# Performance work log

Measured on AMD Instinct MI355X. Metric: run time of the kernel, lower is better.

## Reference

```python
import jax, jax.numpy as jnp
import numpy as np

B, QN, KN, DIN, DPROJ = 8, 2048, 2048, 1024, 1024

def setup_inputs() -> dict:
    key = jax.random.key(0)
    ks = jax.random.split(key, 10)
    s = 1.0 / np.sqrt(DIN)
    return {
        "query": jax.random.normal(ks[0], (B, QN, DIN), jnp.float32),
        "key": jax.random.normal(ks[1], (B, KN, DIN), jnp.float32),
        "value": jax.random.normal(ks[2], (B, KN, DIN), jnp.float32),
        "mask": jax.random.randint(ks[3], (B, KN), 0, 2, jnp.int32),
        "Wq": jax.random.uniform(ks[4], (DPROJ, DIN), jnp.float32, -s, s),
        "bq": jax.random.uniform(ks[5], (DPROJ,), jnp.float32, -s, s),
        "Wk": jax.random.uniform(ks[6], (DPROJ, DIN), jnp.float32, -s, s),
        "bk": jax.random.uniform(ks[7], (DPROJ,), jnp.float32, -s, s),
        "Wv": jax.random.uniform(ks[8], (DPROJ, DIN), jnp.float32, -s, s),
        "bv": jax.random.uniform(ks[9], (DPROJ,), jnp.float32, -s, s),
    }

def reference(query, key, value, mask, Wq, bq, Wk, bk, Wv, bv):
    pq = jnp.einsum('bqc,dc->bqd', query, Wq) + bq  # (b, qn, dproj)
    pk = jnp.einsum('bkc,dc->bkd', key, Wk) + bk    # (b, kn, dproj)
    pv = jnp.einsum('bkc,dc->bkd', value, Wv) + bv  # (b, kn, dproj)
    scores = jnp.einsum('bqd,bkd->bqk', pq, pk) / jnp.sqrt(jnp.float32(DPROJ))
    m = mask[:, None, :]  # (b, 1, kn) broadcasts over qn
    scores = jnp.where(m == 0, jnp.float32(-1e9), scores)
    attn = jax.nn.softmax(scores, axis=-1)
    attn = attn * m.astype(attn.dtype)  # post-softmax double mask
    ctx = jnp.einsum('bqk,bkd->bqd', attn, pv)
    return (ctx, attn)
```

## Files before the change

### kernel.cpp

```cpp
#include <hip/hip_runtime.h>
#include <hip/hip_bf16.h>


typedef __bf16 bf16;
typedef __bf16 bf16x4 __attribute__((ext_vector_type(4)));
typedef __bf16 bf16x8 __attribute__((ext_vector_type(8)));
typedef float f32x4 __attribute__((ext_vector_type(4)));

#define TILE 128
#define BK 32

__device__ __forceinline__ void gld_lds16(const bf16* g, bf16* l) {
  __builtin_amdgcn_global_load_lds(
      (const __attribute__((address_space(1))) void*)g,
      (__attribute__((address_space(3))) void*)l, 16, 0, 0);
}

__global__ __launch_bounds__(256, 2)
void gemm_f32in(const float* __restrict__ A, int lda,
                const float* __restrict__ Bt, int ldb,
                bf16* __restrict__ C, int ldc,
                const float* __restrict__ bias, int bias_mode, int K)
{
  __shared__ bf16 As[TILE * BK];
  __shared__ bf16 Bs[TILE * BK];
  const int tid = threadIdx.x;
  const int wave = tid >> 6, lane = tid & 63;
  const int wm = (wave >> 1) * 64, wn = (wave & 1) * 64;
  const long m0 = (long)blockIdx.x * TILE;
  const long n0 = (long)blockIdx.y * TILE;

  f32x4 acc[4][4] = {};
  const int fr = lane & 15, fq = lane >> 4;

  for (int k0 = 0; k0 < K; k0 += BK) {
    __syncthreads();
#pragma unroll
    for (int j = 0; j < 4; ++j) {
      int c = j * 256 + tid;
      int row = c >> 3, col = (c & 7) * 4;
      f32x4 av = *(const f32x4*)&A[(m0 + row) * (long)lda + k0 + col];
      f32x4 bv = *(const f32x4*)&Bt[(n0 + row) * (long)ldb + k0 + col];
      bf16x4 ab, bb;
      ab[0] = (bf16)av[0]; ab[1] = (bf16)av[1]; ab[2] = (bf16)av[2]; ab[3] = (bf16)av[3];
      bb[0] = (bf16)bv[0]; bb[1] = (bf16)bv[1]; bb[2] = (bf16)bv[2]; bb[3] = (bf16)bv[3];
      *(bf16x4*)&As[row * BK + col] = ab;
      *(bf16x4*)&Bs[row * BK + col] = bb;
    }
    __syncthreads();

    bf16x8 af[4], bg[4];
#pragma unroll
    for (int i = 0; i < 4; ++i)
      af[i] = *(const bf16x8*)&As[(wm + i * 16 + fr) * BK + fq * 8];
#pragma unroll
    for (int i = 0; i < 4; ++i)
      bg[i] = *(const bf16x8*)&Bs[(wn + i * 16 + fr) * BK + fq * 8];
#pragma unroll
    for (int mi = 0; mi < 4; ++mi)
#pragma unroll
      for (int ni = 0; ni < 4; ++ni)
        acc[mi][ni] = __builtin_amdgcn_mfma_f32_16x16x32_bf16(
            af[mi], bg[ni], acc[mi][ni], 0, 0, 0);
  }

  const int cc = lane & 15, cq = lane >> 4;
#pragma unroll
  for (int mi = 0; mi < 4; ++mi)
#pragma unroll
    for (int ni = 0; ni < 4; ++ni)
#pragma unroll
      for (int r = 0; r < 4; ++r) {
        int row = wm + mi * 16 + cq * 4 + r;
        int col = wn + ni * 16 + cc;
        float v = acc[mi][ni][r];
        if (bias_mode == 1) v += bias[n0 + col];
        else if (bias_mode == 2) v += bias[m0 + row];
        C[(m0 + row) * (long)ldc + (n0 + col)] = (bf16)v;
      }
}

__global__ __launch_bounds__(256, 2)
void gemm_bf16(const bf16* __restrict__ A, int lda, long sA,
               const bf16* __restrict__ Bt, int ldb, long sB,
               float* __restrict__ C, int ldc, long sC,
               int K, float scale)
{
  __shared__ bf16 As[TILE * BK];
  __shared__ bf16 Bs[TILE * BK];
  const int tid = threadIdx.x;
  const int wave = tid >> 6, lane = tid & 63;
  const int wm = (wave >> 1) * 64, wn = (wave & 1) * 64;
  const long m0 = (long)blockIdx.x * TILE;
  const long n0 = (long)blockIdx.y * TILE;
  A  += (long)blockIdx.z * sA;
  Bt += (long)blockIdx.z * sB;
  C  += (long)blockIdx.z * sC;

  f32x4 acc[4][4] = {};

  const int srow = tid >> 2;
  const int scol = (tid & 3) * 8;
  const bf16* Ag0 = A  + (m0 + srow) * (long)lda + scol;
  const bf16* Ag1 = A  + (m0 + 64 + srow) * (long)lda + scol;
  const bf16* Bg0 = Bt + (n0 + srow) * (long)ldb + scol;
  const bf16* Bg1 = Bt + (n0 + 64 + srow) * (long)ldb + scol;
  bf16* Al0 = &As[tid * 8];
  bf16* Al1 = &As[(256 + tid) * 8];
  bf16* Bl0 = &Bs[tid * 8];
  bf16* Bl1 = &Bs[(256 + tid) * 8];

  const int fr = lane & 15, fq = lane >> 4;

  for (int k0 = 0; k0 < K; k0 += BK) {
    __syncthreads();
    gld_lds16(Ag0 + k0, Al0);
    gld_lds16(Ag1 + k0, Al1);
    gld_lds16(Bg0 + k0, Bl0);
    gld_lds16(Bg1 + k0, Bl1);
    __syncthreads();

    bf16x8 af[4], bg[4];
#pragma unroll
    for (int i = 0; i < 4; ++i)
      af[i] = *(const bf16x8*)&As[(wm + i * 16 + fr) * BK + fq * 8];
#pragma unroll
    for (int i = 0; i < 4; ++i)
      bg[i] = *(const bf16x8*)&Bs[(wn + i * 16 + fr) * BK + fq * 8];
#pragma unroll
    for (int mi = 0; mi < 4; ++mi)
#pragma unroll
      for (int ni = 0; ni < 4; ++ni)
        acc[mi][ni] = __builtin_amdgcn_mfma_f32_16x16x32_bf16(
            af[mi], bg[ni], acc[mi][ni], 0, 0, 0);
  }

  const int cc = lane & 15, cq = lane >> 4;
#pragma unroll
  for (int mi = 0; mi < 4; ++mi)
#pragma unroll
    for (int ni = 0; ni < 4; ++ni)
#pragma unroll
      for (int r = 0; r < 4; ++r) {
        int row = wm + mi * 16 + cq * 4 + r;
        int col = wn + ni * 16 + cc;
        C[(m0 + row) * (long)ldc + (n0 + col)] = acc[mi][ni][r] * scale;
      }
}

__global__ __launch_bounds__(256)
void softmax_mask(const int* __restrict__ mask, float* __restrict__ attn,
                  bf16* __restrict__ attnb)
{
  const int row = blockIdx.x;
  const int b = row >> 11;
  float* arow = attn + (long)row * 2048;
  bf16* brow = attnb + (long)row * 2048;
  const int* mrow = mask + (b << 11);
  const int tid = threadIdx.x;
  const int lane = tid & 63, wave = tid >> 6;

  f32x4 s[2];
  int4 mk[2];
  s[0] = *(const f32x4*)&arow[tid * 4];
  s[1] = *(const f32x4*)&arow[1024 + tid * 4];
  mk[0] = *(const int4*)&mrow[tid * 4];
  mk[1] = *(const int4*)&mrow[1024 + tid * 4];
  const int m[8] = {mk[0].x, mk[0].y, mk[0].z, mk[0].w,
                    mk[1].x, mk[1].y, mk[1].z, mk[1].w};

  float mx = -3e38f;
#pragma unroll
  for (int i = 0; i < 8; ++i)
    if (m[i]) mx = fmaxf(mx, s[i >> 2][i & 3]);
#pragma unroll
  for (int off = 32; off > 0; off >>= 1) mx = fmaxf(mx, __shfl_xor(mx, off));
  __shared__ float rmax[4], rsum[4];
  if (lane == 0) rmax[wave] = mx;
  __syncthreads();
  mx = fmaxf(fmaxf(rmax[0], rmax[1]), fmaxf(rmax[2], rmax[3]));

  float e[8], sum = 0.f;
#pragma unroll
  for (int i = 0; i < 8; ++i) {
    e[i] = m[i] ? __expf(s[i >> 2][i & 3] - mx) : 0.f;
    sum += e[i];
  }
#pragma unroll
  for (int off = 32; off > 0; off >>= 1) sum += __shfl_xor(sum, off);
  if (lane == 0) rsum[wave] = sum;
  __syncthreads();
  sum = rsum[0] + rsum[1] + rsum[2] + rsum[3];
  float inv = sum > 0.f ? 1.f / sum : 0.f;

  f32x4 o; bf16x4 ob;
#pragma unroll
  for (int h = 0; h < 2; ++h) {
#pragma unroll
    for (int i = 0; i < 4; ++i) {
      float v = e[h * 4 + i] * inv;
      o[i] = v; ob[i] = (bf16)v;
    }
    *(f32x4*)&arow[h * 1024 + tid * 4] = o;
    *(bf16x4*)&brow[h * 1024 + tid * 4] = ob;
  }
}

extern "C" void kernel_launch(void* const* d_in, const int* in_sizes, int n_in,
                              void* d_out, int out_size, void* d_ws, size_t ws_size,
                              hipStream_t stream)
{
  const float* query = (const float*)d_in[0];
  const float* key   = (const float*)d_in[1];
  const float* value = (const float*)d_in[2];
  const int*   mask  = (const int*)d_in[3];
  const float* Wq = (const float*)d_in[4];
  const float* bq = (const float*)d_in[5];
  const float* Wk = (const float*)d_in[6];
  const float* bk = (const float*)d_in[7];
  const float* Wv = (const float*)d_in[8];
  const float* bv = (const float*)d_in[9];

  float* ctx  = (float*)d_out;
  float* attn = ctx + (size_t)8 * 2048 * 1024;

  bf16* Pq    = (bf16*)d_ws;
  bf16* Pk    = Pq + (size_t)16384 * 1024;
  bf16* PvT   = Pk + (size_t)16384 * 1024;
  bf16* attnb = (bf16*)d_ws;

  dim3 blk(256);

  hipLaunchKernelGGL(gemm_f32in, dim3(128, 8), blk, 0, stream,
      query, 1024, Wq, 1024, Pq, 1024, bq, 1, 1024);
  hipLaunchKernelGGL(gemm_f32in, dim3(128, 8), blk, 0, stream,
      key, 1024, Wk, 1024, Pk, 1024, bk, 1, 1024);
  hipLaunchKernelGGL(gemm_f32in, dim3(8, 128), blk, 0, stream,
      Wv, 1024, value, 1024, PvT, 16384, bv, 2, 1024);
  hipLaunchKernelGGL(gemm_bf16, dim3(16, 16, 8), blk, 0, stream,
      Pq, 1024, (long)2048 * 1024, Pk, 1024, (long)2048 * 1024,
      attn, 2048, (long)2048 * 2048, 1024, 0.03125f);
  hipLaunchKernelGGL(softmax_mask, dim3(16384), blk, 0, stream, mask, attn, attnb);
  hipLaunchKernelGGL(gemm_bf16, dim3(16, 8, 8), blk, 0, stream,
      attnb, 2048, (long)2048 * 2048, PvT, 16384, 2048L,
      ctx, 1024, (long)2048 * 1024, 2048, 1.0f);
}
```

Before: 766.0 us.

## Pre-convert weights and value to bf16 and store scores as bf16

Adds a conversion kernel that turns Wq, Wk and value into bf16 once, using the ctx output buffer as scratch. The projection GEMMs then stream the B operand with direct global-to-LDS loads instead of re-reading and converting fp32 in every block. The score GEMM writes bf16 scores into the first half of each fp32 attn row, which softmax reads in place, halving that write and read traffic. Scores are rounded to bf16 before softmax, which costs some precision, and the buffer aliasing relies on each row being read fully before it is overwritten.

```diff
diff --git a/kernel.cpp b/kernel.cpp
--- a/kernel.cpp
+++ b/kernel.cpp
@@ -16,11 +16,24 @@
       (__attribute__((address_space(3))) void*)l, 16, 0, 0);
 }
 
+__global__ __launch_bounds__(256)
+void cvt_f32_bf16(const float* __restrict__ src, bf16* __restrict__ dst, int n)
+{
+  long i = ((long)blockIdx.x * 256 + threadIdx.x) * 8;
+  if (i >= n) return;
+  f32x4 a = *(const f32x4*)&src[i];
+  f32x4 b = *(const f32x4*)&src[i + 4];
+  bf16x8 o;
+  o[0] = (bf16)a[0]; o[1] = (bf16)a[1]; o[2] = (bf16)a[2]; o[3] = (bf16)a[3];
+  o[4] = (bf16)b[0]; o[5] = (bf16)b[1]; o[6] = (bf16)b[2]; o[7] = (bf16)b[3];
+  *(bf16x8*)&dst[i] = o;
+}
+
 __global__ __launch_bounds__(256, 2)
-void gemm_f32in(const float* __restrict__ A, int lda,
-                const float* __restrict__ Bt, int ldb,
-                bf16* __restrict__ C, int ldc,
-                const float* __restrict__ bias, int bias_mode, int K)
+void gemm_af32(const float* __restrict__ A, int lda,
+               const bf16* __restrict__ Bt, int ldb,
+               bf16* __restrict__ C, int ldc,
+               const float* __restrict__ bias, int bias_mode, int K)
 {
   __shared__ bf16 As[TILE * BK];
   __shared__ bf16 Bs[TILE * BK];
@@ -33,19 +46,25 @@
   f32x4 acc[4][4] = {};
   const int fr = lane & 15, fq = lane >> 4;
 
+  const int srow = tid >> 2, scol = (tid & 3) * 8;
+  const bf16* Bg0 = Bt + (n0 + srow) * (long)ldb + scol;
+  const bf16* Bg1 = Bt + (n0 + 64 + srow) * (long)ldb + scol;
+  bf16* Bl0 = &Bs[tid * 8];
+  bf16* Bl1 = &Bs[(256 + tid) * 8];
+
   for (int k0 = 0; k0 < K; k0 += BK) {
     __syncthreads();
+    gld_lds16(Bg0 + k0, Bl0);
+    gld_lds16(Bg1 + k0, Bl1);
 #pragma unroll
     for (int j = 0; j < 4; ++j) {
       int c = j * 256 + tid;
       int row = c >> 3, col = (c & 7) * 4;
       f32x4 av = *(const f32x4*)&A[(m0 + row) * (long)lda + k0 + col];
-      f32x4 bv = *(const f32x4*)&Bt[(n0 + row) * (long)ldb + k0 + col];
-      bf16x4 ab, bb;
-      ab[0] = (bf16)av[0]; ab[1] = (bf16)av[1]; ab[2] = (bf16)av[2]; ab[3] = (bf16)av[3];
-      bb[0] = (bf16)bv[0]; bb[1] = (bf16)bv[1]; bb[2] = (bf16)bv[2]; bb[3] = (bf16)bv[3];
+      bf16x4 ab;
+      ab[0] = (bf16)av[0]; ab[1] = (bf16)av[1];
+      ab[2] = (bf16)av[2]; ab[3] = (bf16)av[3];
       *(bf16x4*)&As[row * BK + col] = ab;
-      *(bf16x4*)&Bs[row * BK + col] = bb;
     }
     __syncthreads();
 
@@ -148,6 +167,73 @@
       }
 }
 
+__global__ __launch_bounds__(256, 2)
+void gemm_score(const bf16* __restrict__ A, int lda, long sA,
+                const bf16* __restrict__ Bt, int ldb, long sB,
+                bf16* __restrict__ C, int K, float scale)
+{
+  __shared__ bf16 As[TILE * BK];
+  __shared__ bf16 Bs[TILE * BK];
+  const int tid = threadIdx.x;
+  const int wave = tid >> 6, lane = tid & 63;
+  const int wm = (wave >> 1) * 64, wn = (wave & 1) * 64;
+  const long m0 = (long)blockIdx.x * TILE;
+  const long n0 = (long)blockIdx.y * TILE;
+  A  += (long)blockIdx.z * sA;
+  Bt += (long)blockIdx.z * sB;
+  C  += (long)blockIdx.z * (2048L * 4096);
+
+  f32x4 acc[4][4] = {};
+
+  const int srow = tid >> 2;
+  const int scol = (tid & 3) * 8;
+  const bf16* Ag0 = A  + (m0 + srow) * (long)lda + scol;
+  const bf16* Ag1 = A  + (m0 + 64 + srow) * (long)lda + scol;
+  const bf16* Bg0 = Bt + (n0 + srow) * (long)ldb + scol;
+  const bf16* Bg1 = Bt + (n0 + 64 + srow) * (long)ldb + scol;
+  bf16* Al0 = &As[tid * 8];
+  bf16* Al1 = &As[(256 + tid) * 8];
+  bf16* Bl0 = &Bs[tid * 8];
+  bf16* Bl1 = &Bs[(256 + tid) * 8];
+
+  const int fr = lane & 15, fq = lane >> 4;
+
+  for (int k0 = 0; k0 < K; k0 += BK) {
+    __syncthreads();
+    gld_lds16(Ag0 + k0, Al0);
+    gld_lds16(Ag1 + k0, Al1);
+    gld_lds16(Bg0 + k0, Bl0);
+    gld_lds16(Bg1 + k0, Bl1);
+    __syncthreads();
+
+    bf16x8 af[4], bg[4];
+#pragma unroll
+    for (int i = 0; i < 4; ++i)
+      af[i] = *(const bf16x8*)&As[(wm + i * 16 + fr) * BK + fq * 8];
+#pragma unroll
+    for (int i = 0; i < 4; ++i)
+      bg[i] = *(const bf16x8*)&Bs[(wn + i * 16 + fr) * BK + fq * 8];
+#pragma unroll
+    for (int mi = 0; mi < 4; ++mi)
+#pragma unroll
+      for (int ni = 0; ni < 4; ++ni)
+        acc[mi][ni] = __builtin_amdgcn_mfma_f32_16x16x32_bf16(
+            af[mi], bg[ni], acc[mi][ni], 0, 0, 0);
+  }
+
+  const int cc = lane & 15, cq = lane >> 4;
+#pragma unroll
+  for (int mi = 0; mi < 4; ++mi)
+#pragma unroll
+    for (int ni = 0; ni < 4; ++ni)
+#pragma unroll
+      for (int r = 0; r < 4; ++r) {
+        int row = wm + mi * 16 + cq * 4 + r;
+        int col = wn + ni * 16 + cc;
+        C[(m0 + row) * 4096L + (n0 + col)] = (bf16)(acc[mi][ni][r] * scale);
+      }
+}
+
 __global__ __launch_bounds__(256)
 void softmax_mask(const int* __restrict__ mask, float* __restrict__ attn,
                   bf16* __restrict__ attnb)
@@ -155,24 +241,28 @@
   const int row = blockIdx.x;
   const int b = row >> 11;
   float* arow = attn + (long)row * 2048;
+  const bf16* srow_b = (const bf16*)arow;
   bf16* brow = attnb + (long)row * 2048;
   const int* mrow = mask + (b << 11);
   const int tid = threadIdx.x;
   const int lane = tid & 63, wave = tid >> 6;
 
-  f32x4 s[2];
+  bf16x4 sb[2];
   int4 mk[2];
-  s[0] = *(const f32x4*)&arow[tid * 4];
-  s[1] = *(const f32x4*)&arow[1024 + tid * 4];
+  sb[0] = *(const bf16x4*)&srow_b[tid * 4];
+  sb[1] = *(const bf16x4*)&srow_b[1024 + tid * 4];
   mk[0] = *(const int4*)&mrow[tid * 4];
   mk[1] = *(const int4*)&mrow[1024 + tid * 4];
   const int m[8] = {mk[0].x, mk[0].y, mk[0].z, mk[0].w,
                     mk[1].x, mk[1].y, mk[1].z, mk[1].w};
+  float s[8];
+#pragma unroll
+  for (int i = 0; i < 8; ++i) s[i] = (float)sb[i >> 2][i & 3];
 
   float mx = -3e38f;
 #pragma unroll
   for (int i = 0; i < 8; ++i)
-    if (m[i]) mx = fmaxf(mx, s[i >> 2][i & 3]);
+    if (m[i]) mx = fmaxf(mx, s[i]);
 #pragma unroll
   for (int off = 32; off > 0; off >>= 1) mx = fmaxf(mx, __shfl_xor(mx, off));
   __shared__ float rmax[4], rsum[4];
@@ -183,7 +273,7 @@
   float e[8], sum = 0.f;
 #pragma unroll
   for (int i = 0; i < 8; ++i) {
-    e[i] = m[i] ? __expf(s[i >> 2][i & 3] - mx) : 0.f;
+    e[i] = m[i] ? __expf(s[i] - mx) : 0.f;
     sum += e[i];
   }
 #pragma unroll
@@ -229,17 +319,26 @@
   bf16* PvT   = Pk + (size_t)16384 * 1024;
   bf16* attnb = (bf16*)d_ws;
 
+  bf16* Wqb = (bf16*)ctx;
+  bf16* Wkb = Wqb + (size_t)1024 * 1024;
+  bf16* vb  = Wkb + (size_t)1024 * 1024;
+
   dim3 blk(256);
 
-  hipLaunchKernelGGL(gemm_f32in, dim3(128, 8), blk, 0, stream,
-      query, 1024, Wq, 1024, Pq, 1024, bq, 1, 1024);
-  hipLaunchKernelGGL(gemm_f32in, dim3(128, 8), blk, 0, stream,
-      key, 1024, Wk, 1024, Pk, 1024, bk, 1, 1024);
-  hipLaunchKernelGGL(gemm_f32in, dim3(8, 128), blk, 0, stream,
-      Wv, 1024, value, 1024, PvT, 16384, bv, 2, 1024);
-  hipLaunchKernelGGL(gemm_bf16, dim3(16, 16, 8), blk, 0, stream,
+  hipLaunchKernelGGL(cvt_f32_bf16, dim3(512), blk, 0, stream, Wq, Wqb, 1024 * 1024);
+  hipLaunchKernelGGL(cvt_f32_bf16, dim3(512), blk, 0, stream, Wk, Wkb, 1024 * 1024);
+  hipLaunchKernelGGL(cvt_f32_bf16, dim3(8192), blk, 0, stream,
+      value, vb, 16384 * 1024);
+
+  hipLaunchKernelGGL(gemm_af32, dim3(128, 8), blk, 0, stream,
+      query, 1024, Wqb, 1024, Pq, 1024, bq, 1, 1024);
+  hipLaunchKernelGGL(gemm_af32, dim3(128, 8), blk, 0, stream,
+      key, 1024, Wkb, 1024, Pk, 1024, bk, 1, 1024);
+  hipLaunchKernelGGL(gemm_af32, dim3(8, 128), blk, 0, stream,
+      Wv, 1024, vb, 1024, PvT, 16384, bv, 2, 1024);
+  hipLaunchKernelGGL(gemm_score, dim3(16, 16, 8), blk, 0, stream,
       Pq, 1024, (long)2048 * 1024, Pk, 1024, (long)2048 * 1024,
-      attn, 2048, (long)2048 * 2048, 1024, 0.03125f);
+      (bf16*)attn, 1024, 0.03125f);
   hipLaunchKernelGGL(softmax_mask, dim3(16384), blk, 0, stream, mask, attn, attnb);
   hipLaunchKernelGGL(gemm_bf16, dim3(16, 8, 8), blk, 0, stream,
       attnb, 2048, (long)2048 * 2048, PvT, 16384, 2048L,
```

Result: faster. 706.9 us (-7.7%).
